# Performance work log

Hardware: AMD Instinct MI355X
Metric: run time of the kernel (lower is better)

## Reference

```python
import jax, jax.numpy as jnp
import numpy as np

VOCAB = 100000
PAD_ID = 0
INTEREST_ID = 1
B, S, D = 16, 200, 128

def setup_inputs() -> dict:
    key = jax.random.key(0)
    ks = jax.random.split(key, 10)
    sc = 0.05
    return {
        "x": jax.random.normal(ks[0], (B, S, D), jnp.float32),
        "x_ids": jax.random.randint(ks[1], (B, S), 0, VOCAB),
        "Wq": jax.random.normal(ks[2], (D, D), jnp.float32) * sc,
        "bq": jax.random.normal(ks[3], (D,), jnp.float32) * sc,
        "Wk": jax.random.normal(ks[4], (D, D), jnp.float32) * sc,
        "bk": jax.random.normal(ks[5], (D,), jnp.float32) * sc,
        "Wv": jax.random.normal(ks[6], (D, 1), jnp.float32) * sc,
        "bv": jax.random.normal(ks[7], (1,), jnp.float32) * sc,
        "Wec": jax.random.normal(ks[8], (2 * D, VOCAB), jnp.float32) * sc,
        "bec": jax.random.normal(ks[9], (VOCAB,), jnp.float32) * sc,
    }

def reference(x, x_ids, Wq, bq, Wk, bk, Wv, bv, Wec, bec):
    # mask: valid (non-pad, non-interest) positions  (B,S)
    mask = (x_ids != PAD_ID) & (x_ids != INTEREST_ID)
    # additive attention pooling (explore_proj=True)
    q = jnp.einsum('bsd,de->bse', x, Wq) + bq            # (B,S,D)
    k = jnp.einsum('bd,de->be', x[:, 0, :], Wk) + bk      # (B,D), broadcast over S
    features = jnp.tanh(q + k[:, None, :])                # (B,S,D)
    scores = jnp.einsum('bsd,do->bso', features, Wv)[..., 0] + bv[0]  # (B,S)
    scores = jax.nn.softmax(scores, axis=-1)
    c_s = jnp.einsum('bsd,bs->bd', x, scores)             # (B,D)
    h_t = x[:, 0, :]                                      # (B,D)
    c_s = jnp.concatenate([h_t, c_s], axis=-1)            # (B,2D)
    p_explore = c_s @ Wec + bec                           # (B,V)
    # explore_mask: histogram of masked ids over vocab.
    # Equivalent to bmm(mask, one_hot(x_ids)) but O(B*S) scatter instead of O(B*S*V).
    explore_mask = jnp.zeros((x.shape[0], VOCAB), jnp.float32)
    batch_idx = jnp.arange(x.shape[0])[:, None]           # (B,1)
    explore_mask = explore_mask.at[batch_idx, x_ids].add(mask.astype(jnp.float32))
    p_explore = jnp.where(explore_mask > 0, -jnp.inf, p_explore)
    return jax.nn.softmax(p_explore, axis=-1)
```

## Files before the change

kernel.cpp:

```cpp
#include <hip/hip_runtime.h>
#include <cstdint>
#include <cstddef>
#include <math.h>

#define B 16
#define S 200
#define D 128
#define VOCAB 100000
#define V4 (VOCAB / 4)
#define SCH 8
#define VTILE 256
#define NBLK ((VOCAB + VTILE - 1) / VTILE)
#define CH 16
#define NCH (2 * D / CH)

__global__ __launch_bounds__(128) void k_scores(
    const float* __restrict__ x,
    const float* __restrict__ Wq, const float* __restrict__ bq,
    const float* __restrict__ Wk, const float* __restrict__ bk,
    const float* __restrict__ Wv, const float* __restrict__ bv,
    float* __restrict__ scores)
{
  const int b  = blockIdx.x / (S / SCH);
  const int s0 = (blockIdx.x % (S / SCH)) * SCH;
  const int e  = threadIdx.x;

  __shared__ float lx[SCH][D];
  __shared__ float l0[D];
  __shared__ float sred[2][SCH];

  l0[e] = x[(size_t)b * S * D + e];
  #pragma unroll
  for (int i = 0; i < SCH; i++) lx[i][e] = x[((size_t)b * S + s0 + i) * D + e];
  __syncthreads();

  float q[SCH];
  const float bqe = bq[e];
  #pragma unroll
  for (int i = 0; i < SCH; i++) q[i] = bqe;
  float kk = bk[e];

  for (int d = 0; d < D; d++) {
    const float wq = Wq[d * D + e];
    const float wk = Wk[d * D + e];
    const float x0 = l0[d];
    kk += x0 * wk;
    #pragma unroll
    for (int i = 0; i < SCH; i++) q[i] += lx[i][d] * wq;
  }

  const float wv  = Wv[e];
  const float bv0 = bv[0];
  #pragma unroll
  for (int i = 0; i < SCH; i++) {
    float val = tanhf(q[i] + kk) * wv;
    #pragma unroll
    for (int off = 32; off > 0; off >>= 1) val += __shfl_down(val, off, 64);
    if ((e & 63) == 0) sred[e >> 6][i] = val;
  }
  __syncthreads();
  if (e < SCH) scores[b * S + s0 + e] = sred[0][e] + sred[1][e] + bv0;
}

__global__ __launch_bounds__(512) void k_csum(
    const float* __restrict__ x, const float* __restrict__ scores,
    float* __restrict__ cvec)
{
  const int b = blockIdx.x;
  const int t = threadIdx.x;
  __shared__ float pr[S];
  __shared__ float redm[9];
  __shared__ float reds[9];
  __shared__ float cpart[3][D];

  float v = (t < S) ? scores[b * S + t] : -INFINITY;
  float m = v;
  #pragma unroll
  for (int off = 32; off > 0; off >>= 1) m = fmaxf(m, __shfl_down(m, off, 64));
  if ((t & 63) == 0) redm[t >> 6] = m;
  __syncthreads();
  if (t == 0) {
    float mm = redm[0];
    #pragma unroll
    for (int i = 1; i < 8; i++) mm = fmaxf(mm, redm[i]);
    redm[8] = mm;
  }
  __syncthreads();
  const float mx = redm[8];

  float e = (t < S) ? expf(v - mx) : 0.f;
  float s = e;
  #pragma unroll
  for (int off = 32; off > 0; off >>= 1) s += __shfl_down(s, off, 64);
  if ((t & 63) == 0) reds[t >> 6] = s;
  __syncthreads();
  if (t == 0) {
    float ss = 0.f;
    #pragma unroll
    for (int i = 0; i < 8; i++) ss += reds[i];
    reds[8] = ss;
  }
  __syncthreads();
  const float inv = 1.0f / reds[8];
  if (t < S) pr[t] = e * inv;
  __syncthreads();

  const int d = t & 127;
  const int sq = t >> 7;
  float acc = 0.f;
  const float* xb = x + ((size_t)b * S + sq * 50) * D + d;
  #pragma unroll 5
  for (int s2 = 0; s2 < 50; s2++) acc += pr[sq * 50 + s2] * xb[s2 * D];
  if (sq) cpart[sq - 1][d] = acc;
  __syncthreads();
  if (sq == 0) {
    cvec[d * B + b]       = x[(size_t)b * S * D + d];
    cvec[(D + d) * B + b] = acc + cpart[0][d] + cpart[1][d] + cpart[2][d];
  }
}

__global__ __launch_bounds__(256, 2) void k_gemv(
    const float* __restrict__ cvec, const float* __restrict__ Wec,
    const float* __restrict__ bec, const int* __restrict__ ids,
    float* __restrict__ out, float* __restrict__ partial)
{
  __shared__ __align__(16) char arena[49152];
  float (*wbuf)[CH][VTILE] = (float (*)[CH][VTILE])arena;
  float* cl = (float*)(arena + 32768);
  __shared__ unsigned mbit[B * 8];

  const int t    = threadIdx.x;
  const int lane = t & 63;
  const int dq   = __builtin_amdgcn_readfirstlane(t >> 6);

  {
    const float4* src = (const float4*)cvec;
    float4* dst = (float4*)cl;
    #pragma unroll
    for (int i = 0; i < 4; i++) dst[t + 256 * i] = src[t + 256 * i];
  }
  if (t < B * 8) mbit[t] = 0u;

  const int vbase = blockIdx.x * VTILE;
  const int v4    = blockIdx.x * 64 + lane;
  const bool valid = (v4 < V4);
  const int v4c   = valid ? v4 : (V4 - 1);
  const int laneoff = (vbase + lane * 4 + 3 < VOCAB) ? lane * 4 : 0;

#define STAGE(bufi, c)                                                      \
  { _Pragma("unroll")                                                       \
    for (int r = 0; r < 4; r++) {                                           \
      const int d = (c) * CH + dq * 4 + r;                                  \
      const float* gp = Wec + (size_t)d * VOCAB + vbase + laneoff;          \
      float* lp = &wbuf[bufi][dq * 4 + r][0];                               \
      __builtin_amdgcn_global_load_lds(                                     \
          (const __attribute__((address_space(1))) void*)gp,                \
          (__attribute__((address_space(3))) void*)lp, 16, 0, 0);           \
    } }

  float4 acc[16];
  #pragma unroll
  for (int i = 0; i < 16; i++) acc[i] = make_float4(0.f, 0.f, 0.f, 0.f);

  STAGE(0, 0)

  for (int i = t; i < B * S; i += 256) {
    const int id = ids[i];
    if (id > 1 && id >= vbase && id < vbase + VTILE) {
      const int lv = id - vbase;
      atomicOr(&mbit[(i / S) * 8 + (lv >> 5)], 1u << (lv & 31));
    }
  }

  __syncthreads();

  int cur = 0;
  for (int c = 0; c < NCH; c++) {
    if (c < NCH - 1) STAGE(cur ^ 1, c + 1)
    #pragma unroll
    for (int r = 0; r < 4; r++) {
      const float4 w = ((const float4*)&wbuf[cur][dq * 4 + r][0])[lane];
      const float* cj = cl + (c * CH + dq * 4 + r) * 16;
      #pragma unroll
      for (int bb = 0; bb < 16; bb++) {
        const float cc = cj[bb];
        acc[bb].x = fmaf(w.x, cc, acc[bb].x);
        acc[bb].y = fmaf(w.y, cc, acc[bb].y);
        acc[bb].z = fmaf(w.z, cc, acc[bb].z);
        acc[bb].w = fmaf(w.w, cc, acc[bb].w);
      }
    }
    __syncthreads();
    cur ^= 1;
  }
#undef STAGE

  float2* redp = (float2*)arena;
#define RED(q, l, b) redp[(((q) * 64 + (l)) * 17) + (b)]
#define MASKED(bb, lv) ((mbit[(bb) * 8 + ((lv) >> 5)] >> ((lv) & 31)) & 1u)

  const float4 be4 = ((const float4*)bec)[v4c];
  const int lv0 = lane * 4;
  float psum[4] = {0.f, 0.f, 0.f, 0.f};

  #pragma unroll
  for (int bb = 0; bb < 16; bb++)
    RED(dq, lane, bb) = make_float2(acc[bb].x, acc[bb].y);
  __syncthreads();
  #pragma unroll
  for (int i = 0; i < 4; i++) {
    const int bb = dq * 4 + i;
    const float2 r0 = RED(0, lane, bb), r1 = RED(1, lane, bb);
    const float2 r2 = RED(2, lane, bb), r3 = RED(3, lane, bb);
    const float sx = r0.x + r1.x + r2.x + r3.x;
    const float sy = r0.y + r1.y + r2.y + r3.y;
    float e0 = 0.f, e1 = 0.f;
    if (valid) {
      e0 = MASKED(bb, lv0 + 0) ? 0.f : __expf(sx + be4.x);
      e1 = MASKED(bb, lv0 + 1) ? 0.f : __expf(sy + be4.y);
      *(float2*)&out[(size_t)bb * VOCAB + (size_t)v4 * 4] = make_float2(e0, e1);
    }
    psum[i] += e0 + e1;
  }
  __syncthreads();

  #pragma unroll
  for (int bb = 0; bb < 16; bb++)
    RED(dq, lane, bb) = make_float2(acc[bb].z, acc[bb].w);
  __syncthreads();
  #pragma unroll
  for (int i = 0; i < 4; i++) {
    const int bb = dq * 4 + i;
    const float2 r0 = RED(0, lane, bb), r1 = RED(1, lane, bb);
    const float2 r2 = RED(2, lane, bb), r3 = RED(3, lane, bb);
    const float sz = r0.x + r1.x + r2.x + r3.x;
    const float sw = r0.y + r1.y + r2.y + r3.y;
    float e2 = 0.f, e3 = 0.f;
    if (valid) {
      e2 = MASKED(bb, lv0 + 2) ? 0.f : __expf(sz + be4.z);
      e3 = MASKED(bb, lv0 + 3) ? 0.f : __expf(sw + be4.w);
      *(float2*)&out[(size_t)bb * VOCAB + (size_t)v4 * 4 + 2] = make_float2(e2, e3);
    }
    psum[i] += e2 + e3;
  }
#undef RED
#undef MASKED

  #pragma unroll
  for (int i = 0; i < 4; i++) {
    float s = psum[i];
    #pragma unroll
    for (int off = 32; off > 0; off >>= 1) s += __shfl_down(s, off, 64);
    if (lane == 0) partial[blockIdx.x * 16 + dq * 4 + i] = s;
  }
}

__global__ __launch_bounds__(256) void k_norm(float* __restrict__ out,
                                              const float* __restrict__ partial)
{
  const int b  = blockIdx.y;
  const int t  = threadIdx.x;
  __shared__ float red[4];

  float s = 0.f;
  for (int j = t; j < NBLK; j += 256) s += partial[j * 16 + b];
  #pragma unroll
  for (int off = 32; off > 0; off >>= 1) s += __shfl_down(s, off, 64);
  if ((t & 63) == 0) red[t >> 6] = s;
  __syncthreads();
  const float iv = 1.0f / (red[0] + red[1] + red[2] + red[3]);

  const int i4 = blockIdx.x * 256 + t;
  if (i4 < V4) {
    float4* p = (float4*)out + (size_t)b * V4 + i4;
    float4 q = *p;
    q.x *= iv; q.y *= iv; q.z *= iv; q.w *= iv;
    *p = q;
  }
}

extern "C" void kernel_launch(void* const* d_in, const int* in_sizes, int n_in,
                              void* d_out, int out_size, void* d_ws, size_t ws_size,
                              hipStream_t stream)
{
  const float* x   = (const float*)d_in[0];
  const int*   ids = (const int*)d_in[1];
  const float* Wq  = (const float*)d_in[2];
  const float* bq  = (const float*)d_in[3];
  const float* Wk  = (const float*)d_in[4];
  const float* bk  = (const float*)d_in[5];
  const float* Wv  = (const float*)d_in[6];
  const float* bv  = (const float*)d_in[7];
  const float* Wec = (const float*)d_in[8];
  const float* bec = (const float*)d_in[9];
  float* out = (float*)d_out;
  float* ws  = (float*)d_ws;

  float* scores  = ws;
  float* cvec    = ws + 3200;
  float* partial = ws + 7296;

  k_scores <<<dim3(B * (S / SCH)), dim3(128), 0, stream>>>(x, Wq, bq, Wk, bk, Wv, bv, scores);
  k_csum   <<<dim3(B),             dim3(512), 0, stream>>>(x, scores, cvec);
  k_gemv   <<<dim3(NBLK),          dim3(256), 0, stream>>>(cvec, Wec, bec, ids, out, partial);
  k_norm   <<<dim3((V4 + 255) / 256, B), dim3(256), 0, stream>>>(out, partial);
}
```

Measured before the change: 57.27 us.

## Triple-buffer Wec staging with per-wave vmcnt waits instead of block barriers

The GEMV over Wec moves from double buffering with a `__syncthreads` per chunk to a three-buffer ring. Two chunks are prefetched ahead through global_load_lds, and each wave waits on its own loads with explicit `s_waitcnt vmcnt`. This works because every wave stages and consumes only its own rows. The shared copy of the context vector moves to a separate shared array so the full arena can hold three buffers. The aim is to keep more HBM traffic in flight and remove per-chunk block-wide synchronisation. The cost is more LDS per block, which could limit occupancy, and the scheme depends on hand-counted vmcnt values being correct.

```diff
diff --git a/kernel.cpp b/kernel.cpp
--- a/kernel.cpp
+++ b/kernel.cpp
@@ -126,19 +126,13 @@
 {
   __shared__ __align__(16) char arena[49152];
   float (*wbuf)[CH][VTILE] = (float (*)[CH][VTILE])arena;
-  float* cl = (float*)(arena + 32768);
+  __shared__ __align__(16) float cl[4096];
   __shared__ unsigned mbit[B * 8];
 
   const int t    = threadIdx.x;
   const int lane = t & 63;
   const int dq   = __builtin_amdgcn_readfirstlane(t >> 6);
 
-  {
-    const float4* src = (const float4*)cvec;
-    float4* dst = (float4*)cl;
-    #pragma unroll
-    for (int i = 0; i < 4; i++) dst[t + 256 * i] = src[t + 256 * i];
-  }
   if (t < B * 8) mbit[t] = 0u;
 
   const int vbase = blockIdx.x * VTILE;
@@ -158,11 +152,33 @@
           (__attribute__((address_space(3))) void*)lp, 16, 0, 0);           \
     } }
 
+#define COMP(bufi, c)                                                      \
+  { _Pragma("unroll")                                                      \
+    for (int r = 0; r < 4; r++) {                                          \
+      const float4 w = ((const float4*)&wbuf[bufi][dq * 4 + r][0])[lane];  \
+      const float* cj = cl + ((c) * CH + dq * 4 + r) * 16;                 \
+      _Pragma("unroll")                                                    \
+      for (int bb = 0; bb < 16; bb++) {                                    \
+        const float cc = cj[bb];                                           \
+        acc[bb].x = fmaf(w.x, cc, acc[bb].x);                              \
+        acc[bb].y = fmaf(w.y, cc, acc[bb].y);                              \
+        acc[bb].z = fmaf(w.z, cc, acc[bb].z);                              \
+        acc[bb].w = fmaf(w.w, cc, acc[bb].w);                              \
+      } } }
+
   float4 acc[16];
   #pragma unroll
   for (int i = 0; i < 16; i++) acc[i] = make_float4(0.f, 0.f, 0.f, 0.f);
 
+  {
+    const float4* src = (const float4*)cvec;
+    float4* dst = (float4*)cl;
+    #pragma unroll
+    for (int i = 0; i < 4; i++) dst[t + 256 * i] = src[t + 256 * i];
+  }
+
   STAGE(0, 0)
+  STAGE(1, 1)
 
   for (int i = t; i < B * S; i += 256) {
     const int id = ids[i];
@@ -174,26 +190,24 @@
 
   __syncthreads();
 
-  int cur = 0;
-  for (int c = 0; c < NCH; c++) {
-    if (c < NCH - 1) STAGE(cur ^ 1, c + 1)
-    #pragma unroll
-    for (int r = 0; r < 4; r++) {
-      const float4 w = ((const float4*)&wbuf[cur][dq * 4 + r][0])[lane];
-      const float* cj = cl + (c * CH + dq * 4 + r) * 16;
-      #pragma unroll
-      for (int bb = 0; bb < 16; bb++) {
-        const float cc = cj[bb];
-        acc[bb].x = fmaf(w.x, cc, acc[bb].x);
-        acc[bb].y = fmaf(w.y, cc, acc[bb].y);
-        acc[bb].z = fmaf(w.z, cc, acc[bb].z);
-        acc[bb].w = fmaf(w.w, cc, acc[bb].w);
-      }
-    }
-    __syncthreads();
-    cur ^= 1;
-  }
+  for (int c = 0; c < NCH - 2; c++) {
+    STAGE((c + 2) % 3, c + 2)
+    asm volatile("s_waitcnt vmcnt(8)" ::: "memory");
+    __builtin_amdgcn_sched_barrier(0);
+    COMP(c % 3, c)
+    __builtin_amdgcn_sched_barrier(0);
+  }
+  asm volatile("s_waitcnt vmcnt(4)" ::: "memory");
+  __builtin_amdgcn_sched_barrier(0);
+  COMP((NCH - 2) % 3, NCH - 2)
+  asm volatile("s_waitcnt vmcnt(0)" ::: "memory");
+  __builtin_amdgcn_sched_barrier(0);
+  COMP((NCH - 1) % 3, NCH - 1)
+
 #undef STAGE
+#undef COMP
+
+  __syncthreads();
 
   float2* redp = (float2*)arena;
 #define RED(q, l, b) redp[(((q) * 64 + (l)) * 17) + (b)]
```

New measurement: 56.21 us. About the same (-1.8%).

## Split GEMV by batch across waves with direct global weight loads

Applied to the files above, without the earlier changes.

Each wave of the vocab GEMV kernel now owns four batch rows over the full 256-deep reduction instead of a quarter of the depth for all sixteen rows. This removes the double-buffered LDS staging of Wec, the per-chunk barriers and the cross-wave LDS reduction. Weights are read straight from global memory into registers in batches of sixteen float4 loads, and occupancy is raised to four blocks per CU. In exchange, each Wec element is loaded by all four waves instead of one, which quadruples weight load traffic and leans on L1/L2 hits.

```diff
diff --git a/kernel.cpp b/kernel.cpp
--- a/kernel.cpp
+++ b/kernel.cpp
@@ -11,8 +11,6 @@
 #define SCH 8
 #define VTILE 256
 #define NBLK ((VOCAB + VTILE - 1) / VTILE)
-#define CH 16
-#define NCH (2 * D / CH)
 
 __global__ __launch_bounds__(128) void k_scores(
     const float* __restrict__ x,
@@ -119,19 +117,17 @@
   }
 }
 
-__global__ __launch_bounds__(256, 2) void k_gemv(
+__global__ __launch_bounds__(256, 4) void k_gemv(
     const float* __restrict__ cvec, const float* __restrict__ Wec,
     const float* __restrict__ bec, const int* __restrict__ ids,
     float* __restrict__ out, float* __restrict__ partial)
 {
-  __shared__ __align__(16) char arena[49152];
-  float (*wbuf)[CH][VTILE] = (float (*)[CH][VTILE])arena;
-  float* cl = (float*)(arena + 32768);
+  __shared__ __align__(16) float cl[256 * 16];
   __shared__ unsigned mbit[B * 8];
 
   const int t    = threadIdx.x;
   const int lane = t & 63;
-  const int dq   = __builtin_amdgcn_readfirstlane(t >> 6);
+  const int bq   = t >> 6;
 
   {
     const float4* src = (const float4*)cvec;
@@ -145,24 +141,8 @@
   const int v4    = blockIdx.x * 64 + lane;
   const bool valid = (v4 < V4);
   const int v4c   = valid ? v4 : (V4 - 1);
-  const int laneoff = (vbase + lane * 4 + 3 < VOCAB) ? lane * 4 : 0;
-
-#define STAGE(bufi, c)                                                      \
-  { _Pragma("unroll")                                                       \
-    for (int r = 0; r < 4; r++) {                                           \
-      const int d = (c) * CH + dq * 4 + r;                                  \
-      const float* gp = Wec + (size_t)d * VOCAB + vbase + laneoff;          \
-      float* lp = &wbuf[bufi][dq * 4 + r][0];                               \
-      __builtin_amdgcn_global_load_lds(                                     \
-          (const __attribute__((address_space(1))) void*)gp,                \
-          (__attribute__((address_space(3))) void*)lp, 16, 0, 0);           \
-    } }
-
-  float4 acc[16];
-  #pragma unroll
-  for (int i = 0; i < 16; i++) acc[i] = make_float4(0.f, 0.f, 0.f, 0.f);
-
-  STAGE(0, 0)
+
+  const float4* wp = (const float4*)Wec + v4c;
 
   for (int i = t; i < B * S; i += 256) {
     const int id = ids[i];
@@ -171,88 +151,60 @@
       atomicOr(&mbit[(i / S) * 8 + (lv >> 5)], 1u << (lv & 31));
     }
   }
-
-  __syncthreads();
-
-  int cur = 0;
-  for (int c = 0; c < NCH; c++) {
-    if (c < NCH - 1) STAGE(cur ^ 1, c + 1)
-    #pragma unroll
-    for (int r = 0; r < 4; r++) {
-      const float4 w = ((const float4*)&wbuf[cur][dq * 4 + r][0])[lane];
-      const float* cj = cl + (c * CH + dq * 4 + r) * 16;
-      #pragma unroll
-      for (int bb = 0; bb < 16; bb++) {
-        const float cc = cj[bb];
-        acc[bb].x = fmaf(w.x, cc, acc[bb].x);
-        acc[bb].y = fmaf(w.y, cc, acc[bb].y);
-        acc[bb].z = fmaf(w.z, cc, acc[bb].z);
-        acc[bb].w = fmaf(w.w, cc, acc[bb].w);
-      }
+  __syncthreads();
+
+  float4 acc[4];
+  #pragma unroll
+  for (int i = 0; i < 4; i++) acc[i] = make_float4(0.f, 0.f, 0.f, 0.f);
+
+  for (int c = 0; c < 16; c++) {
+    float4 w[16];
+    #pragma unroll
+    for (int j = 0; j < 16; j++)
+      w[j] = wp[(size_t)(c * 16 + j) * V4];
+    #pragma unroll
+    for (int j = 0; j < 16; j++) {
+      const float4 cb = *(const float4*)&cl[(c * 16 + j) * 16 + bq * 4];
+      acc[0].x = fmaf(w[j].x, cb.x, acc[0].x);
+      acc[0].y = fmaf(w[j].y, cb.x, acc[0].y);
+      acc[0].z = fmaf(w[j].z, cb.x, acc[0].z);
+      acc[0].w = fmaf(w[j].w, cb.x, acc[0].w);
+      acc[1].x = fmaf(w[j].x, cb.y, acc[1].x);
+      acc[1].y = fmaf(w[j].y, cb.y, acc[1].y);
+      acc[1].z = fmaf(w[j].z, cb.y, acc[1].z);
+      acc[1].w = fmaf(w[j].w, cb.y, acc[1].w);
+      acc[2].x = fmaf(w[j].x, cb.z, acc[2].x);
+      acc[2].y = fmaf(w[j].y, cb.z, acc[2].y);
+      acc[2].z = fmaf(w[j].z, cb.z, acc[2].z);
+      acc[2].w = fmaf(w[j].w, cb.z, acc[2].w);
+      acc[3].x = fmaf(w[j].x, cb.w, acc[3].x);
+      acc[3].y = fmaf(w[j].y, cb.w, acc[3].y);
+      acc[3].z = fmaf(w[j].z, cb.w, acc[3].z);
+      acc[3].w = fmaf(w[j].w, cb.w, acc[3].w);
     }
-    __syncthreads();
-    cur ^= 1;
-  }
-#undef STAGE
-
-  float2* redp = (float2*)arena;
-#define RED(q, l, b) redp[(((q) * 64 + (l)) * 17) + (b)]
+  }
+
 #define MASKED(bb, lv) ((mbit[(bb) * 8 + ((lv) >> 5)] >> ((lv) & 31)) & 1u)
-
   const float4 be4 = ((const float4*)bec)[v4c];
   const int lv0 = lane * 4;
-  float psum[4] = {0.f, 0.f, 0.f, 0.f};
-
-  #pragma unroll
-  for (int bb = 0; bb < 16; bb++)
-    RED(dq, lane, bb) = make_float2(acc[bb].x, acc[bb].y);
-  __syncthreads();
+
   #pragma unroll
   for (int i = 0; i < 4; i++) {
-    const int bb = dq * 4 + i;
-    const float2 r0 = RED(0, lane, bb), r1 = RED(1, lane, bb);
-    const float2 r2 = RED(2, lane, bb), r3 = RED(3, lane, bb);
-    const float sx = r0.x + r1.x + r2.x + r3.x;
-    const float sy = r0.y + r1.y + r2.y + r3.y;
-    float e0 = 0.f, e1 = 0.f;
+    const int bb = bq * 4 + i;
+    float4 e = make_float4(0.f, 0.f, 0.f, 0.f);
     if (valid) {
-      e0 = MASKED(bb, lv0 + 0) ? 0.f : __expf(sx + be4.x);
-      e1 = MASKED(bb, lv0 + 1) ? 0.f : __expf(sy + be4.y);
-      *(float2*)&out[(size_t)bb * VOCAB + (size_t)v4 * 4] = make_float2(e0, e1);
+      e.x = MASKED(bb, lv0 + 0) ? 0.f : __expf(acc[i].x + be4.x);
+      e.y = MASKED(bb, lv0 + 1) ? 0.f : __expf(acc[i].y + be4.y);
+      e.z = MASKED(bb, lv0 + 2) ? 0.f : __expf(acc[i].z + be4.z);
+      e.w = MASKED(bb, lv0 + 3) ? 0.f : __expf(acc[i].w + be4.w);
+      *(float4*)&out[(size_t)bb * VOCAB + (size_t)v4 * 4] = e;
     }
-    psum[i] += e0 + e1;
-  }
-  __syncthreads();
-
-  #pragma unroll
-  for (int bb = 0; bb < 16; bb++)
-    RED(dq, lane, bb) = make_float2(acc[bb].z, acc[bb].w);
-  __syncthreads();
-  #pragma unroll
-  for (int i = 0; i < 4; i++) {
-    const int bb = dq * 4 + i;
-    const float2 r0 = RED(0, lane, bb), r1 = RED(1, lane, bb);
-    const float2 r2 = RED(2, lane, bb), r3 = RED(3, lane, bb);
-    const float sz = r0.x + r1.x + r2.x + r3.x;
-    const float sw = r0.y + r1.y + r2.y + r3.y;
-    float e2 = 0.f, e3 = 0.f;
-    if (valid) {
-      e2 = MASKED(bb, lv0 + 2) ? 0.f : __expf(sz + be4.z);
-      e3 = MASKED(bb, lv0 + 3) ? 0.f : __expf(sw + be4.w);
-      *(float2*)&out[(size_t)bb * VOCAB + (size_t)v4 * 4 + 2] = make_float2(e2, e3);
-    }
-    psum[i] += e2 + e3;
-  }
-#undef RED
+    float s = e.x + e.y + e.z + e.w;
+    #pragma unroll
+    for (int off = 32; off > 0; off >>= 1) s += __shfl_down(s, off, 64);
+    if (lane == 0) partial[blockIdx.x * 16 + bb] = s;
+  }
 #undef MASKED
-
-  #pragma unroll
-  for (int i = 0; i < 4; i++) {
-    float s = psum[i];
-    #pragma unroll
-    for (int off = 32; off > 0; off >>= 1) s += __shfl_down(s, off, 64);
-    if (lane == 0) partial[blockIdx.x * 16 + dq * 4 + i] = s;
-  }
 }
 
 __global__ __launch_bounds__(256) void k_norm(float* __restrict__ out,
```

Result: slower. 82.56 us (+44.2%).
